# Performance work log

Measured on AMD Instinct MI355X. Metric: run time of the kernel, lower is better.

Reference implementation:

```python
import jax, jax.numpy as jnp
import numpy as np

EMB_DIM = 1024
N_HEAD = 16
HEAD_SIZE = 64
B = 2
T = 2048


def setup_inputs() -> dict:
    key = jax.random.key(0)
    k_x, k_qkv, k_pw, k_pb = jax.random.split(key, 4)
    x = jax.random.normal(k_x, (B, T, EMB_DIM), dtype=jnp.float32)
    # nn.Linear(emb_dim, 3*emb_dim, bias=False): y = x @ W_qkv, W_qkv: [C, 3C]
    W_qkv = jax.random.normal(k_qkv, (EMB_DIM, 3 * EMB_DIM), dtype=jnp.float32) * (EMB_DIM ** -0.5)
    # nn.Linear(emb_dim, emb_dim) with bias
    W_proj = jax.random.normal(k_pw, (EMB_DIM, EMB_DIM), dtype=jnp.float32) * (EMB_DIM ** -0.5)
    b_proj = jax.random.normal(k_pb, (EMB_DIM,), dtype=jnp.float32) * 0.01
    return {"x": x, "W_qkv": W_qkv, "W_proj": W_proj, "b_proj": b_proj}


def reference(x, W_qkv, W_proj, b_proj):
    Bn, Tn, C = x.shape
    qkv = x @ W_qkv                          # [B, T, 3C]
    q, k, v = jnp.split(qkv, 3, axis=-1)
    # [B, T, H, D] -> attention over heads via einsum (no explicit transpose)
    q = q.reshape(Bn, Tn, N_HEAD, HEAD_SIZE)
    k = k.reshape(Bn, Tn, N_HEAD, HEAD_SIZE)
    v = v.reshape(Bn, Tn, N_HEAD, HEAD_SIZE)
    att = jnp.einsum("bthd,bshd->bhts", q, k) * (HEAD_SIZE ** -0.5)  # [B, H, T, T]
    causal = jnp.tril(jnp.ones((Tn, Tn), dtype=bool))
    att = jnp.where(causal, att, -jnp.inf)
    att = jax.nn.softmax(att, axis=-1)
    y = jnp.einsum("bhts,bshd->bthd", att, v).reshape(Bn, Tn, C)
    return y @ W_proj + b_proj
```

## Files before the change

### kernel.cpp

```cpp
#include <hip/hip_runtime.h>
#include <hip/hip_bf16.h>

typedef unsigned short u16;
typedef unsigned int u32;
typedef u16 u16x4 __attribute__((ext_vector_type(4)));
typedef u16 u16x8 __attribute__((ext_vector_type(8)));
typedef u32 u32x4 __attribute__((ext_vector_type(4)));
typedef __bf16 bf16x8 __attribute__((ext_vector_type(8)));
typedef float f32x4 __attribute__((ext_vector_type(4)));

__device__ __forceinline__ u16 f2bf(float f) {
  union { float f; unsigned u; } v; v.f = f;
  unsigned r = v.u + 0x7fffu + ((v.u >> 16) & 1u);
  return (u16)(r >> 16);
}

__device__ __forceinline__ u16 bf(float f) {
  __bf16 h = (__bf16)f;
  union { __bf16 h; u16 u; } c; c.h = h;
  return c.u;
}

__device__ __forceinline__ u32 pack2(float lo, float hi) {
  return (u32)bf(lo) | ((u32)bf(hi) << 16);
}

__device__ __forceinline__ float fexp2(float x) {
#if __has_builtin(__builtin_amdgcn_exp2f)
  return __builtin_amdgcn_exp2f(x);
#else
  return exp2f(x);
#endif
}

__device__ __forceinline__ float frcp(float x) {
#if __has_builtin(__builtin_amdgcn_rcpf)
  return __builtin_amdgcn_rcpf(x);
#else
  return 1.0f / x;
#endif
}

__device__ __forceinline__ void gload16(const void* g, void* l) {
  __builtin_amdgcn_global_load_lds((const __attribute__((address_space(1))) void*)g,
                                   (__attribute__((address_space(3))) void*)l, 16, 0, 0);
}

__global__ __launch_bounds__(256) void prep(
    const float* __restrict__ x, const float* __restrict__ Wqkv,
    const float* __restrict__ Wproj, u16* __restrict__ xb,
    u16* __restrict__ wqT, u16* __restrict__ wpT)
{
  __shared__ float tile[32][33];
  const int bid = blockIdx.x;
  if (bid < 2048) {
    int i = (bid * 256 + threadIdx.x) * 8;
    f32x4 a = *(const f32x4*)(x + i);
    f32x4 b = *(const f32x4*)(x + i + 4);
    u16x8 r;
    r[0] = f2bf(a[0]); r[1] = f2bf(a[1]); r[2] = f2bf(a[2]); r[3] = f2bf(a[3]);
    r[4] = f2bf(b[0]); r[5] = f2bf(b[1]); r[6] = f2bf(b[2]); r[7] = f2bf(b[3]);
    *(u16x8*)(xb + i) = r;
    return;
  }
  int flat = bid - 2048;
  int bx = flat & 127, by = flat >> 7;
  const float* in;
  u16* out;
  int N;
  if (bx < 96) { in = Wqkv; out = wqT; N = 3072; }
  else         { in = Wproj; out = wpT; N = 1024; bx -= 96; }
  const int K = 1024;
  int n0 = bx * 32, k0 = by * 32;
  int tx = threadIdx.x & 31, ty = threadIdx.x >> 5;
  for (int i = 0; i < 32; i += 8)
    tile[ty + i][tx] = in[(long)(k0 + ty + i) * N + n0 + tx];
  __syncthreads();
  for (int i = 0; i < 32; i += 8)
    out[(long)(n0 + ty + i) * K + k0 + tx] = f2bf(tile[tx][ty + i]);
}

template<int BM, int BN, bool F32OUT>
__global__ __launch_bounds__(256) void gemm_bt(
    const u16* __restrict__ A, const u16* __restrict__ Bt,
    void* __restrict__ Cp, const float* __restrict__ bias,
    int M, int N, int K)
{
  constexpr int MR = BM / 32, NR = BN / 32;
  constexpr int RA = BM / 32, RB = BN / 32;
  __shared__ char lds[(BM + BN) * 128];
  char* As = lds;
  char* Bs = lds + BM * 128;
  const int tid = threadIdx.x;
  const int l = tid & 63, w = tid >> 6;
  const int wr = w >> 1, wc = w & 1;
  const int lr = l & 15, q4 = l >> 4;
  const long row0 = (long)blockIdx.x * BM;
  const long col0 = (long)blockIdx.y * BN;

  f32x4 acc[MR][NR] = {};

  const u16* gA[RA];
  int oA[RA];
  for (int i = 0; i < RA; ++i) {
    int cc = i * 256 + tid;
    int r = cc >> 3, c = (cc & 7) ^ (r & 7);
    oA[i] = cc * 16;
    gA[i] = A + (row0 + r) * K + c * 8;
  }
  const u16* gB[RB];
  int oB[RB];
  for (int i = 0; i < RB; ++i) {
    int cc = i * 256 + tid;
    int r = cc >> 3, c = (cc & 7) ^ (r & 7);
    oB[i] = cc * 16;
    gB[i] = Bt + (col0 + r) * K + c * 8;
  }

  for (int k0 = 0; k0 < K; k0 += 64) {
    __syncthreads();
    for (int i = 0; i < RA; ++i) gload16(gA[i] + k0, As + oA[i]);
    for (int i = 0; i < RB; ++i) gload16(gB[i] + k0, Bs + oB[i]);
    __syncthreads();
    for (int kk = 0; kk < 2; ++kk) {
      bf16x8 a[MR], b[NR];
      for (int m = 0; m < MR; ++m) {
        int r = wr * (BM / 2) + m * 16 + lr;
        a[m] = *(const bf16x8*)(As + r * 128 + (((kk * 4 + q4) ^ (r & 7)) << 4));
      }
      for (int n = 0; n < NR; ++n) {
        int r = wc * (BN / 2) + n * 16 + lr;
        b[n] = *(const bf16x8*)(Bs + r * 128 + (((kk * 4 + q4) ^ (r & 7)) << 4));
      }
      for (int m = 0; m < MR; ++m)
        for (int n = 0; n < NR; ++n)
          acc[m][n] = __builtin_amdgcn_mfma_f32_16x16x32_bf16(a[m], b[n], acc[m][n], 0, 0, 0);
    }
  }

  for (int n = 0; n < NR; ++n) {
    int col = (int)col0 + wc * (BN / 2) + n * 16 + lr;
    float bv = 0.f;
    if (F32OUT) bv = bias[col];
    for (int m = 0; m < MR; ++m) {
      for (int reg = 0; reg < 4; ++reg) {
        long row = row0 + wr * (BM / 2) + m * 16 + q4 * 4 + reg;
        float vv = acc[m][n][reg] + bv;
        if (F32OUT) ((float*)Cp)[row * N + col] = vv;
        else        ((u16*)Cp)[row * N + col] = f2bf(vv);
      }
    }
  }
}

#define FXOR(d) (((((d) & 7) ^ (((d) >> 3) & 7))) << 4)

#define VSCAT(vtb, ra, rb)                                                     \
  for (int j = 0; j < 4; ++j) {                                                \
    int d = vd0 + j;                                                           \
    *(u32*)((vtb) + d * 128 + (vcol2 ^ FXOR(d))) = (u32)(ra)[j] | ((u32)(rb)[j] << 16); \
  }

#define COMPUTE_TILE(T)                                                        \
  if (64 * (T) <= wrow + 15) {                                                 \
    char* ks_ = ksmem + ((T) & 3) * 8192;                                      \
    char* vt_ = vtmem + ((T) & 3) * 8192;                                      \
    const int k0_ = 64 * (T);                                                  \
    f32x4 st[4] = {};                                                          \
    __builtin_amdgcn_s_setprio(1);                                             \
    for (int kk = 0; kk < 2; ++kk)                                             \
      for (int n = 0; n < 4; ++n) {                                            \
        int r = n * 16 + lr;                                                   \
        int c = (kk * 4 + g) ^ (r & 7);                                        \
        bf16x8 kf = *(const bf16x8*)(ks_ + r * 128 + (c << 4));                \
        st[n] = __builtin_amdgcn_mfma_f32_16x16x32_bf16(kf, qf[kk], st[n], 0, 0, 0); \
      }                                                                        \
    __builtin_amdgcn_s_setprio(0);                                             \
    if (k0_ + 63 > wrow) {                                                     \
      for (int n = 0; n < 4; ++n)                                              \
        for (int reg = 0; reg < 4; ++reg)                                      \
          if (k0_ + n * 16 + g * 4 + reg > wrow + lr)                          \
            st[n][reg] = -__builtin_inff();                                    \
    }                                                                          \
    float psum = 0.f;                                                          \
    u32 pk[4][2];                                                              \
    for (int n = 0; n < 4; ++n) {                                              \
      float p0 = fexp2(st[n][0]), p1 = fexp2(st[n][1]);                        \
      float p2 = fexp2(st[n][2]), p3 = fexp2(st[n][3]);                        \
      psum += (p0 + p1) + (p2 + p3);                                           \
      pk[n][0] = pack2(p0, p1);                                                \
      pk[n][1] = pack2(p2, p3);                                                \
    }                                                                          \
    lsum += psum;                                                              \
    __builtin_amdgcn_s_setprio(1);                                             \
    for (int kt = 0; kt < 2; ++kt) {                                           \
      u32x4 pb;                                                                \
      pb[0] = pk[2 * kt][0]; pb[1] = pk[2 * kt][1];                            \
      pb[2] = pk[2 * kt + 1][0]; pb[3] = pk[2 * kt + 1][1];                    \
      bf16x8 pf = *(bf16x8*)&pb;                                               \
      for (int n = 0; n < 4; ++n) {                                            \
        int dd = n * 16 + lr;                                                  \
        bf16x8 vf = *(const bf16x8*)(vt_ + dd * 128 + ((kt * 64 + g * 16) ^ FXOR(dd))); \
        o[n] = __builtin_amdgcn_mfma_f32_16x16x32_bf16(vf, pf, o[n], 0, 0, 0); \
      }                                                                        \
    }                                                                          \
    __builtin_amdgcn_s_setprio(0);                                             \
  }

__global__ __launch_bounds__(512) void attn_fwd(
    const u16* __restrict__ qkv, u16* __restrict__ atty)
{
  __shared__ char ksmem[4 * 8192];
  __shared__ char vtmem[4 * 8192];
  const int tid = threadIdx.x;
  const int l = tid & 63, w = tid >> 6;
  const int lr = l & 15, g = l >> 4;
  const int h = blockIdx.y;
  const int ti = blockIdx.x;
  const long base = (long)blockIdx.z * 2048;
  const int wrow = (w < 4) ? (ti * 64 + w * 16) : ((31 - ti) * 64 + (w - 4) * 16);

  bf16x8 qf[2];
  for (int kk = 0; kk < 2; ++kk) {
    u16x8 raw = *(const u16x8*)(qkv + (base + wrow + lr) * 3072 + h * 64 + kk * 32 + g * 8);
    u16x8 sc;
    for (int j = 0; j < 8; ++j) {
      union { unsigned u; float f; } c; c.u = ((unsigned)raw[j]) << 16;
      sc[j] = bf(c.f * 0.18033688f);
    }
    qf[kk] = *(bf16x8*)&sc;
  }

  float lsum = 0.f;
  f32x4 o[4] = {};

  const int kr = tid >> 3, kc = (tid & 7) ^ (kr & 7);
  const u16* kg = qkv + (base + kr) * 3072 + 1024 + h * 64 + kc * 8;
  const int va = tid >> 4;
  const int vd0 = (tid & 15) * 4;
  const int vk0 = va * 2;
  const int vn = vk0 >> 4, vgp2 = (vk0 >> 2) & 3, vr = vk0 & 3;
  const int vcol2 = ((vn >> 1) * 32 + vgp2 * 8 + (vn & 1) * 4 + vr) * 2;
  const u16* vgp = qkv + (base + vk0) * 3072 + 2048 + h * 64 + vd0;

  const int nkv = 32 - ti;

  {
    u16x4 a0 = *(const u16x4*)(vgp);
    u16x4 b0 = *(const u16x4*)(vgp + 3072);
    u16x4 a1 = *(const u16x4*)(vgp + 196608);
    u16x4 b1 = *(const u16x4*)(vgp + 196608 + 3072);
    gload16(kg, ksmem + tid * 16);
    gload16(kg + 196608, ksmem + 8192 + tid * 16);
    VSCAT(vtmem, a0, b0);
    VSCAT(vtmem + 8192, a1, b1);
  }
  __syncthreads();

  for (int tb = 0; tb < nkv; tb += 2) {
    u16x4 p2a, p2b, p3a, p3b;
    const bool pf2 = (tb + 2) < nkv, pf3 = (tb + 3) < nkv;
    if (pf2) {
      long off = (long)(tb + 2) * 196608;
      p2a = *(const u16x4*)(vgp + off);
      p2b = *(const u16x4*)(vgp + off + 3072);
      gload16(kg + off, ksmem + ((tb + 2) & 3) * 8192 + tid * 16);
    }
    if (pf3) {
      long off = (long)(tb + 3) * 196608;
      p3a = *(const u16x4*)(vgp + off);
      p3b = *(const u16x4*)(vgp + off + 3072);
      gload16(kg + off, ksmem + ((tb + 3) & 3) * 8192 + tid * 16);
    }

    COMPUTE_TILE(tb);
    if (tb + 1 < nkv) COMPUTE_TILE(tb + 1);

    if (pf2) VSCAT(vtmem + ((tb + 2) & 3) * 8192, p2a, p2b);
    if (pf3) VSCAT(vtmem + ((tb + 3) & 3) * 8192, p3a, p3b);
    __syncthreads();
  }

  lsum += __shfl_xor(lsum, 16);
  lsum += __shfl_xor(lsum, 32);
  float inv = frcp(lsum);
  long row = base + wrow + lr;
  for (int n = 0; n < 4; ++n) {
    u16x4 ov;
    for (int reg = 0; reg < 4; ++reg) ov[reg] = bf(o[n][reg] * inv);
    *(u16x4*)(atty + row * 1024 + h * 64 + n * 16 + g * 4) = ov;
  }
}

extern "C" void kernel_launch(void* const* d_in, const int* in_sizes, int n_in,
                              void* d_out, int out_size, void* d_ws, size_t ws_size,
                              hipStream_t stream) {
  const float* x     = (const float*)d_in[0];
  const float* Wqkv  = (const float*)d_in[1];
  const float* Wproj = (const float*)d_in[2];
  const float* bproj = (const float*)d_in[3];
  char* ws = (char*)d_ws;
  u16* xb   = (u16*)(ws);
  u16* wqT  = (u16*)(ws + 8388608);
  u16* wpT  = (u16*)(ws + 14680064);
  u16* qkv  = (u16*)(ws + 16777216);
  u16* atty = (u16*)(ws + 41943040);

  prep<<<6144, 256, 0, stream>>>(x, Wqkv, Wproj, xb, wqT, wpT);
  gemm_bt<128, 192, false><<<dim3(32, 16), 256, 0, stream>>>(xb, wqT, (void*)qkv, nullptr, 4096, 3072, 1024);
  attn_fwd<<<dim3(16, 16, 2), 512, 0, stream>>>(qkv, atty);
  gemm_bt<128, 64, true><<<dim3(32, 16), 256, 0, stream>>>(atty, wpT, d_out, bproj, 4096, 1024, 1024);
}
```

Baseline: 104.5 us.

## Balance causal attention work between wave groups by splitting the high query tile's KV range

Before, waves 0-3 handled the low query tile (few KV tiles) and waves 4-7 the high tile (many KV tiles), so half the block sat idle in later iterations. Now waves 4-7 process the first 16 KV tiles for the high tile. Waves 0-3 process the low tile's tiles and then the remaining high-tile tiles. Partial outputs and row sums are merged through shared memory at the end. This evens out per-wave MFMA work at the cost of a second set of Q fragments and accumulators, a reduction step, and a changed staging and slot schedule.

```diff
diff --git a/kernel.cpp b/kernel.cpp
--- a/kernel.cpp
+++ b/kernel.cpp
@@ -161,11 +161,10 @@
     *(u32*)((vtb) + d * 128 + (vcol2 ^ FXOR(d))) = (u32)(ra)[j] | ((u32)(rb)[j] << 16); \
   }
 
-#define COMPUTE_TILE(T)                                                        \
-  if (64 * (T) <= wrow + 15) {                                                 \
-    char* ks_ = ksmem + ((T) & 3) * 8192;                                      \
-    char* vt_ = vtmem + ((T) & 3) * 8192;                                      \
-    const int k0_ = 64 * (T);                                                  \
+#define CTILE(QF, OACC, LS, SLOT, K0, ROW, DOMASK)                             \
+  {                                                                            \
+    char* ks_ = ksmem + (SLOT) * 8192;                                         \
+    char* vt_ = vtmem + (SLOT) * 8192;                                         \
     f32x4 st[4] = {};                                                          \
     __builtin_amdgcn_s_setprio(1);                                             \
     for (int kk = 0; kk < 2; ++kk)                                             \
@@ -173,13 +172,13 @@
         int r = n * 16 + lr;                                                   \
         int c = (kk * 4 + g) ^ (r & 7);                                        \
         bf16x8 kf = *(const bf16x8*)(ks_ + r * 128 + (c << 4));                \
-        st[n] = __builtin_amdgcn_mfma_f32_16x16x32_bf16(kf, qf[kk], st[n], 0, 0, 0); \
+        st[n] = __builtin_amdgcn_mfma_f32_16x16x32_bf16(kf, QF[kk], st[n], 0, 0, 0); \
       }                                                                        \
     __builtin_amdgcn_s_setprio(0);                                             \
-    if (k0_ + 63 > wrow) {                                                     \
+    if (DOMASK) {                                                              \
       for (int n = 0; n < 4; ++n)                                              \
         for (int reg = 0; reg < 4; ++reg)                                      \
-          if (k0_ + n * 16 + g * 4 + reg > wrow + lr)                          \
+          if ((K0) + n * 16 + g * 4 + reg > (ROW) + lr)                        \
             st[n][reg] = -__builtin_inff();                                    \
     }                                                                          \
     float psum = 0.f;                                                          \
@@ -191,7 +190,7 @@
       pk[n][0] = pack2(p0, p1);                                                \
       pk[n][1] = pack2(p2, p3);                                                \
     }                                                                          \
-    lsum += psum;                                                              \
+    LS += psum;                                                                \
     __builtin_amdgcn_s_setprio(1);                                             \
     for (int kt = 0; kt < 2; ++kt) {                                           \
       u32x4 pb;                                                                \
@@ -201,7 +200,7 @@
       for (int n = 0; n < 4; ++n) {                                            \
         int dd = n * 16 + lr;                                                  \
         bf16x8 vf = *(const bf16x8*)(vt_ + dd * 128 + ((kt * 64 + g * 16) ^ FXOR(dd))); \
-        o[n] = __builtin_amdgcn_mfma_f32_16x16x32_bf16(vf, pf, o[n], 0, 0, 0); \
+        OACC[n] = __builtin_amdgcn_mfma_f32_16x16x32_bf16(vf, pf, OACC[n], 0, 0, 0); \
       }                                                                        \
     }                                                                          \
     __builtin_amdgcn_s_setprio(0);                                             \
@@ -218,21 +217,35 @@
   const int h = blockIdx.y;
   const int ti = blockIdx.x;
   const long base = (long)blockIdx.z * 2048;
-  const int wrow = (w < 4) ? (ti * 64 + w * 16) : ((31 - ti) * 64 + (w - 4) * 16);
-
-  bf16x8 qf[2];
+  const bool isA = w < 4;
+  const int wq = w & 3;
+  const int lorow = ti * 64 + wq * 16;
+  const int hirow = (31 - ti) * 64 + wq * 16;
+
+  bf16x8 qfH[2], qfL[2];
   for (int kk = 0; kk < 2; ++kk) {
-    u16x8 raw = *(const u16x8*)(qkv + (base + wrow + lr) * 3072 + h * 64 + kk * 32 + g * 8);
+    u16x8 raw = *(const u16x8*)(qkv + (base + hirow + lr) * 3072 + h * 64 + kk * 32 + g * 8);
     u16x8 sc;
     for (int j = 0; j < 8; ++j) {
       union { unsigned u; float f; } c; c.u = ((unsigned)raw[j]) << 16;
       sc[j] = bf(c.f * 0.18033688f);
     }
-    qf[kk] = *(bf16x8*)&sc;
-  }
-
-  float lsum = 0.f;
-  f32x4 o[4] = {};
+    qfH[kk] = *(bf16x8*)&sc;
+  }
+  if (isA) {
+    for (int kk = 0; kk < 2; ++kk) {
+      u16x8 raw = *(const u16x8*)(qkv + (base + lorow + lr) * 3072 + h * 64 + kk * 32 + g * 8);
+      u16x8 sc;
+      for (int j = 0; j < 8; ++j) {
+        union { unsigned u; float f; } c; c.u = ((unsigned)raw[j]) << 16;
+        sc[j] = bf(c.f * 0.18033688f);
+      }
+      qfL[kk] = *(bf16x8*)&sc;
+    }
+  }
+
+  float ls_hi = 0.f, ls_lo = 0.f;
+  f32x4 o_hi[4] = {}, o_lo[4] = {};
 
   const int kr = tid >> 3, kc = (tid & 7) ^ (kr & 7);
   const u16* kg = qkv + (base + kr) * 3072 + 1024 + h * 64 + kc * 8;
@@ -243,51 +256,71 @@
   const int vcol2 = ((vn >> 1) * 32 + vgp2 * 8 + (vn & 1) * 4 + vr) * 2;
   const u16* vgp = qkv + (base + vk0) * 3072 + 2048 + h * 64 + vd0;
 
-  const int nkv = 32 - ti;
-
   {
     u16x4 a0 = *(const u16x4*)(vgp);
     u16x4 b0 = *(const u16x4*)(vgp + 3072);
-    u16x4 a1 = *(const u16x4*)(vgp + 196608);
-    u16x4 b1 = *(const u16x4*)(vgp + 196608 + 3072);
-    gload16(kg, ksmem + tid * 16);
-    gload16(kg + 196608, ksmem + 8192 + tid * 16);
-    VSCAT(vtmem, a0, b0);
-    VSCAT(vtmem + 8192, a1, b1);
+    gload16(kg, ksmem + 2 * 8192 + tid * 16);
+    VSCAT(vtmem + 2 * 8192, a0, b0);
   }
   __syncthreads();
 
-  for (int tb = 0; tb < nkv; tb += 2) {
-    u16x4 p2a, p2b, p3a, p3b;
-    const bool pf2 = (tb + 2) < nkv, pf3 = (tb + 3) < nkv;
-    if (pf2) {
-      long off = (long)(tb + 2) * 196608;
-      p2a = *(const u16x4*)(vgp + off);
-      p2b = *(const u16x4*)(vgp + off + 3072);
-      gload16(kg + off, ksmem + ((tb + 2) & 3) * 8192 + tid * 16);
-    }
-    if (pf3) {
-      long off = (long)(tb + 3) * 196608;
-      p3a = *(const u16x4*)(vgp + off);
-      p3b = *(const u16x4*)(vgp + off + 3072);
-      gload16(kg + off, ksmem + ((tb + 3) & 3) * 8192 + tid * 16);
-    }
-
-    COMPUTE_TILE(tb);
-    if (tb + 1 < nkv) COMPUTE_TILE(tb + 1);
-
-    if (pf2) VSCAT(vtmem + ((tb + 2) & 3) * 8192, p2a, p2b);
-    if (pf3) VSCAT(vtmem + ((tb + 3) & 3) * 8192, p3a, p3b);
+  for (int u = 0; u <= 16; ++u) {
+    const bool stB = (u + 1) <= 15;
+    const bool stA = ((u + 1) > ti) && ((u + 1) <= 16);
+    const int sB = 2 + ((u + 1) & 1);
+    const int sA = (u + 1) & 1;
+    u16x4 bva, bvb, ava, avb;
+    if (stB) {
+      long off = (long)(u + 1) * 196608;
+      bva = *(const u16x4*)(vgp + off);
+      bvb = *(const u16x4*)(vgp + off + 3072);
+      gload16(kg + off, ksmem + sB * 8192 + tid * 16);
+    }
+    if (stA) {
+      long off = (long)(u + 16 - ti) * 196608;
+      ava = *(const u16x4*)(vgp + off);
+      avb = *(const u16x4*)(vgp + off + 3072);
+      gload16(kg + off, ksmem + sA * 8192 + tid * 16);
+    }
+
+    if (isA) {
+      if (u <= ti) {
+        CTILE(qfL, o_lo, ls_lo, 2 + (u & 1), 64 * u, lorow, u == ti);
+      } else {
+        CTILE(qfH, o_hi, ls_hi, u & 1, 64 * (u + 15 - ti), hirow, u == 16);
+      }
+    } else if (u <= 15) {
+      CTILE(qfH, o_hi, ls_hi, 2 + (u & 1), 64 * u, hirow, false);
+    }
+
+    if (stB) VSCAT(vtmem + sB * 8192, bva, bvb);
+    if (stA) VSCAT(vtmem + sA * 8192, ava, avb);
     __syncthreads();
   }
 
-  lsum += __shfl_xor(lsum, 16);
-  lsum += __shfl_xor(lsum, 32);
-  float inv = frcp(lsum);
-  long row = base + wrow + lr;
+  float* sh = (float*)ksmem;
+  const int bofs = (wq * 64 + l) * 17;
+  if (isA) {
+    for (int n = 0; n < 4; ++n)
+      for (int r = 0; r < 4; ++r) sh[bofs + n * 4 + r] = o_hi[n][r];
+    sh[bofs + 16] = ls_hi;
+  }
+  __syncthreads();
+  long row;
+  if (isA) {
+    row = base + lorow + lr;
+  } else {
+    for (int n = 0; n < 4; ++n)
+      for (int r = 0; r < 4; ++r) o_lo[n][r] = o_hi[n][r] + sh[bofs + n * 4 + r];
+    ls_lo = ls_hi + sh[bofs + 16];
+    row = base + hirow + lr;
+  }
+  ls_lo += __shfl_xor(ls_lo, 16);
+  ls_lo += __shfl_xor(ls_lo, 32);
+  float inv = frcp(ls_lo);
   for (int n = 0; n < 4; ++n) {
     u16x4 ov;
-    for (int reg = 0; reg < 4; ++reg) ov[reg] = bf(o[n][reg] * inv);
+    for (int reg = 0; reg < 4; ++reg) ov[reg] = bf(o_lo[n][reg] * inv);
     *(u16x4*)(atty + row * 1024 + h * 64 + n * 16 + g * 4) = ov;
   }
 }
```

After: 111.8 us. 7.0% more time.
